# Kernel optimization log

Hardware: AMD Instinct MI355X
Metric: run time of the kernel (lower is better)

Reference implementation:

```python
import jax, jax.numpy as jnp
import numpy as np

B, L, D, H, NL = 4, 2048, 128, 4, 2
DH = D // H
FF = 2 * D
EPS_LN = 1e-5


def _p(key, shape, scale=0.05):
    return (jax.random.normal(key, shape, dtype=jnp.float32) * scale)


def setup_inputs() -> dict:
    key = jax.random.key(0)
    ks = jax.random.split(key, 40)
    inp = {
        "local_global": jax.random.normal(ks[0], (B, D), dtype=jnp.float32),
        "task_features": jax.random.normal(ks[1], (B, L, 15), dtype=jnp.float32),
        "privacy_features": jax.random.normal(ks[2], (B, L, 6), dtype=jnp.float32),
        "dag_features": jax.random.normal(ks[3], (B, L, 4), dtype=jnp.float32),
        # float mask in [0,1); values > 0.5 are MASKED (set to -inf) per torch code
        "attn_mask": jax.random.uniform(ks[4], (B, L, L), dtype=jnp.float32),
        # input projections (stored [in, out]; torch Linear does x @ W.T + b)
        "task_W": _p(ks[5], (15, D)), "task_b": jnp.zeros((D,), jnp.float32),
        "priv_W": _p(ks[6], (6, D)), "priv_b": jnp.zeros((D,), jnp.float32),
        "dag_W": _p(ks[7], (4, D)), "dag_b": jnp.zeros((D,), jnp.float32),
        "pre_g": jnp.ones((D,), jnp.float32), "pre_b": jnp.zeros((D,), jnp.float32),
        "post_g": jnp.ones((D,), jnp.float32), "post_b": jnp.zeros((D,), jnp.float32),
        "out_W": _p(ks[8], (D, D)), "out_b": jnp.zeros((D,), jnp.float32),
        # per-layer params stacked on leading NL axis
        "qW": _p(ks[9], (NL, D, D)), "qb": jnp.zeros((NL, D), jnp.float32),
        "kW": _p(ks[10], (NL, D, D)), "kb": jnp.zeros((NL, D), jnp.float32),
        "vW": _p(ks[11], (NL, D, D)), "vb": jnp.zeros((NL, D), jnp.float32),
        "oW": _p(ks[12], (NL, D, D)), "ob": jnp.zeros((NL, D), jnp.float32),
        "n1g": jnp.ones((NL, D), jnp.float32), "n1b": jnp.zeros((NL, D), jnp.float32),
        "n2g": jnp.ones((NL, D), jnp.float32), "n2b": jnp.zeros((NL, D), jnp.float32),
        "f1W": _p(ks[13], (NL, D, FF)), "f1b": jnp.zeros((NL, FF), jnp.float32),
        "f2W": _p(ks[14], (NL, FF, D)), "f2b": jnp.zeros((NL, D), jnp.float32),
    }
    return inp


def _layernorm(x, g, b):
    mu = x.mean(-1, keepdims=True)
    var = ((x - mu) ** 2).mean(-1, keepdims=True)
    return (x - mu) * jax.lax.rsqrt(var + EPS_LN) * g + b


def _attention(x, add_mask, Wq, bq, Wk, bk, Wv, bv, Wo, bo):
    # x: [B,L,D]; add_mask: [B,L,L] additive (0 or -inf)
    def heads(y):
        return y.reshape(B, L, H, DH).transpose(0, 2, 1, 3)  # [B,H,L,DH]
    q = heads(x @ Wq + bq)
    k = heads(x @ Wk + bk)
    v = heads(x @ Wv + bv)
    scale = 1.0 / np.sqrt(DH).astype(np.float32)
    scores = jnp.einsum('bhqd,bhkd->bhqk', q, k) * scale + add_mask[:, None]
    # fully-masked-row diagonal fixup (torch: set diag score to 0 where row max is -inf)
    row_max = scores.max(-1)                       # [B,H,L]
    fully_masked = jnp.isinf(row_max) & (row_max < 0)
    eye = jnp.eye(L, dtype=bool)
    scores = jnp.where(fully_masked[..., None] & eye, 0.0, scores)
    w = jax.nn.softmax(scores, axis=-1)
    # NaN fallback: if any NaN, replace with 1/L and renormalize (applied globally, as torch does)
    has_nan = jnp.isnan(w).any()
    fixed = jnp.nan_to_num(w, nan=1.0 / L)
    fixed = fixed / (fixed.sum(-1, keepdims=True) + 1e-8)
    w = jnp.where(has_nan, fixed, w)
    out = jnp.einsum('bhqk,bhkd->bhqd', w, v)      # [B,H,L,DH]
    out = out.transpose(0, 2, 1, 3).reshape(B, L, D)
    return out @ Wo + bo


def reference(local_global, task_features, privacy_features, dag_features, attn_mask,
              task_W, task_b, priv_W, priv_b, dag_W, dag_b,
              pre_g, pre_b, post_g, post_b, out_W, out_b,
              qW, qb, kW, kb, vW, vb, oW, ob,
              n1g, n1b, n2g, n2b, f1W, f1b, f2W, f2b):
    # normalize mask: >0.5 means masked; fix all-False rows by masking their diagonal (torch quirk)
    mb = attn_mask > 0.5                            # [B,L,L] bool, True = mask out
    need_fix = ~mb.any(-1)                          # [B,L]
    eye = jnp.eye(L, dtype=bool)
    mb = mb | (need_fix[..., None] & eye)
    add_mask = jnp.where(mb, -jnp.inf, 0.0).astype(jnp.float32)

    ctx = (task_features @ task_W + task_b) + (privacy_features @ priv_W + priv_b) \
          + (dag_features @ dag_W + dag_b)
    x = _layernorm(ctx, pre_g, pre_b)
    for i in range(NL):  # eval mode: dropout = identity
        sa = _attention(_layernorm(x, n1g[i], n1b[i]), add_mask,
                        qW[i], qb[i], kW[i], kb[i], vW[i], vb[i], oW[i], ob[i])
        x = x + sa
        h = _layernorm(x, n2g[i], n2b[i])
        ff = jax.nn.gelu(h @ f1W[i] + f1b[i], approximate=False) @ f2W[i] + f2b[i]
        x = x + ff
    enc = _layernorm(x, post_g, post_b)
    global_ctx = enc.mean(axis=1)                   # [B,D]
    fused = global_ctx + 0.1 * local_global
    aligned = fused @ out_W + out_b
    return aligned
```

## Files before the change

### kernel.cpp

```cpp
#include <hip/hip_runtime.h>
#include <hip/hip_bf16.h>

#define DEV __device__ __forceinline__

typedef float f32x4 __attribute__((ext_vector_type(4)));
typedef float f32x16 __attribute__((ext_vector_type(16)));
typedef short s16x8 __attribute__((ext_vector_type(8)));
typedef unsigned short u16x4 __attribute__((ext_vector_type(4)));
typedef __bf16 bf16x8 __attribute__((ext_vector_type(8)));

DEV bf16x8 as_bf16(s16x8 v) { return __builtin_bit_cast(bf16x8, v); }

DEV unsigned short f2bf(float f) {
    union { __hip_bfloat16 h; unsigned short u; } c;
    c.h = __float2bfloat16(f);
    return c.u;
}

DEV unsigned f2bf2(float lo, float hi) {
    unsigned ulo = __builtin_bit_cast(unsigned, lo);
    unsigned uhi = __builtin_bit_cast(unsigned, hi);
    ulo = (ulo + 0x7fffu + ((ulo >> 16) & 1u)) >> 16;
    uhi = (uhi + 0x7fffu + ((uhi >> 16) & 1u)) & 0xffff0000u;
    return ulo | uhi;
}

DEV float wave_sum64(float v) {
#pragma unroll
    for (int m = 1; m < 64; m <<= 1) v += __shfl_xor(v, m, 64);
    return v;
}

DEV int rot3(int r) { return ((r << 1) | (r >> 2)) & 7; }

constexpr float QSCL = (float)(1.4426950408889634 / 5.656854249492381);

__global__ __launch_bounds__(256) void gace_setup_k(
    const float* __restrict__ am, unsigned long long* __restrict__ bits,
    const float* __restrict__ task, const float* __restrict__ priv, const float* __restrict__ dag,
    const float* __restrict__ tW, const float* __restrict__ tb,
    const float* __restrict__ pW, const float* __restrict__ pb,
    const float* __restrict__ dW, const float* __restrict__ db,
    const float* __restrict__ pre_g, const float* __restrict__ pre_b,
    float* __restrict__ x,
    const float* __restrict__ qW, const float* __restrict__ kW,
    const float* __restrict__ vW, const float* __restrict__ oW,
    const float* __restrict__ f1W, const float* __restrict__ f2W,
    const float* __restrict__ qb, const float* __restrict__ kb,
    const float* __restrict__ vb,
    unsigned short* __restrict__ wbf, float* __restrict__ bcat)
{
    const int bx = blockIdx.x;
    const int tid = threadIdx.x, wid = tid >> 6, l = tid & 63;
    if (bx < 2048) {
        const int row = bx * 4 + wid;
        const float* mrow = am + (size_t)row * 2048;
        unsigned long long myword = 0, orAll = 0, andAll = ~0ull;
#pragma unroll 4
        for (int w = 0; w < 32; ++w) {
            unsigned long long bal = __ballot(mrow[w * 64 + l] > 0.5f);
            if (w == l) myword = bal;
            orAll |= bal; andAll &= bal;
        }
        const int lrow = row & 2047;
        const int dw = lrow >> 6, dbit = lrow & 63;
        if (l == dw) {
            if (orAll == 0ull) myword |= (1ull << dbit);
            else if (andAll == ~0ull) myword &= ~(1ull << dbit);
        }
        if (l < 32) bits[(size_t)row * 32 + l] = myword;
        return;
    }
    if (bx < 4096) {
        const int row = (bx - 2048) * 4 + wid;
        const int d0 = l, d1 = l + 64;
        float a0 = tb[d0] + pb[d0] + db[d0];
        float a1 = tb[d1] + pb[d1] + db[d1];
        const float* tf = task + (size_t)row * 15;
#pragma unroll
        for (int j = 0; j < 15; ++j) { const float t = tf[j]; a0 += t * tW[j * 128 + d0]; a1 += t * tW[j * 128 + d1]; }
        const float* pf = priv + (size_t)row * 6;
#pragma unroll
        for (int j = 0; j < 6; ++j) { const float t = pf[j]; a0 += t * pW[j * 128 + d0]; a1 += t * pW[j * 128 + d1]; }
        const float* df = dag + (size_t)row * 4;
#pragma unroll
        for (int j = 0; j < 4; ++j) { const float t = df[j]; a0 += t * dW[j * 128 + d0]; a1 += t * dW[j * 128 + d1]; }
        const float s = wave_sum64(a0 + a1);
        const float mean = s * (1.f / 128.f);
        const float e0 = a0 - mean, e1 = a1 - mean;
        const float s2 = wave_sum64(e0 * e0 + e1 * e1);
        const float rs = rsqrtf(s2 * (1.f / 128.f) + 1e-5f);
        x[(size_t)row * 128 + d0] = e0 * rs * pre_g[d0] + pre_b[d0];
        x[(size_t)row * 128 + d1] = e1 * rs * pre_g[d1] + pre_b[d1];
        return;
    }
    const int bx2 = bx - 4096;
    const int y = bx2 >> 8;
    const int idx = (bx2 & 255) * 256 + tid;
    if (y == 6) {
        if (idx < 2 * 384) {
            const int i = idx / 384, j = idx % 384;
            float v;
            if (j < 128)      v = qb[i * 128 + j] * QSCL;
            else if (j < 256) v = kb[i * 128 + j - 128];
            else              v = vb[i * 128 + j - 256];
            bcat[idx] = v;
        }
        return;
    }
    const float* src; int K_, N_, off; float scl = 1.0f;
    switch (y) {
        case 0:  src = qW;  K_ = 128; N_ = 128; off = 0;      scl = QSCL; break;
        case 1:  src = kW;  K_ = 128; N_ = 128; off = 16384;  break;
        case 2:  src = vW;  K_ = 128; N_ = 128; off = 32768;  break;
        case 3:  src = oW;  K_ = 128; N_ = 128; off = 49152;  break;
        case 4:  src = f1W; K_ = 128; N_ = 256; off = 65536;  break;
        default: src = f2W; K_ = 256; N_ = 128; off = 98304;  break;
    }
    const int per = K_ * N_;
    if (idx >= 2 * per) return;
    const int i = idx / per, rem = idx % per;
    const int n = rem / K_, k = rem % K_;
    wbf[(size_t)i * 131072 + off + n * K_ + k] = f2bf(src[(size_t)i * per + k * N_ + n] * scl);
}

template<int PRO, int EPI, int KD>
__global__ __launch_bounds__(256) void gace_mega_k(
    const unsigned short* __restrict__ A, int lda,
    const float* __restrict__ xin,
    const float* __restrict__ Op, const float* __restrict__ ml,
    const float* __restrict__ gam, const float* __restrict__ bet,
    const unsigned short* __restrict__ Wt,
    const float* __restrict__ bias,
    unsigned short* __restrict__ outb, int ldo,
    float* __restrict__ xadd, unsigned short* __restrict__ vtbuf)
{
    const int tid = threadIdx.x;
    const int wid = tid >> 6, l = tid & 63;
    const int g = (l >> 4) & 3, c16 = l & 15;
    const int m0 = blockIdx.x * 64 + wid * 16;
    const int n0 = blockIdx.y * 64;
    const int arow = m0 + c16;
    constexpr int NKC = KD / 32;

    s16x8 af[NKC];
    if (PRO == 0) {
#pragma unroll
        for (int kc = 0; kc < NKC; ++kc)
            af[kc] = *(const s16x8*)&A[(size_t)arow * lda + kc * 32 + 8 * g];
    } else if (PRO == 1) {
        float v[4][8];
#pragma unroll
        for (int kc = 0; kc < 4; ++kc) {
            const f32x4 a0 = *(const f32x4*)&xin[(size_t)arow * 128 + kc * 32 + 8 * g];
            const f32x4 a1 = *(const f32x4*)&xin[(size_t)arow * 128 + kc * 32 + 8 * g + 4];
#pragma unroll
            for (int e = 0; e < 4; ++e) { v[kc][e] = a0[e]; v[kc][4 + e] = a1[e]; }
        }
        float s = 0.f;
#pragma unroll
        for (int kc = 0; kc < 4; ++kc)
#pragma unroll
            for (int e = 0; e < 8; ++e) s += v[kc][e];
        s += __shfl_xor(s, 16, 64); s += __shfl_xor(s, 32, 64);
        const float mean = s * (1.f / 128.f);
        float s2 = 0.f;
#pragma unroll
        for (int kc = 0; kc < 4; ++kc)
#pragma unroll
            for (int e = 0; e < 8; ++e) { const float d = v[kc][e] - mean; s2 += d * d; }
        s2 += __shfl_xor(s2, 16, 64); s2 += __shfl_xor(s2, 32, 64);
        const float rs = rsqrtf(s2 * (1.f / 128.f) + 1e-5f);
#pragma unroll
        for (int kc = 0; kc < 4; ++kc) {
            union { s16x8 v8; unsigned d[4]; } pk;
#pragma unroll
            for (int j = 0; j < 4; ++j) {
                const int col = kc * 32 + 8 * g + 2 * j;
                const float x0 = (v[kc][2 * j] - mean) * rs * gam[col] + bet[col];
                const float x1 = (v[kc][2 * j + 1] - mean) * rs * gam[col + 1] + bet[col + 1];
                pk.d[j] = f2bf2(x0, x1);
            }
            af[kc] = pk.v8;
        }
    } else {
#pragma unroll
        for (int kc = 0; kc < 4; ++kc) {
            float o[8];
#pragma unroll
            for (int e = 0; e < 8; ++e) o[e] = 0.f;
            float Ls = 0.f;
#pragma unroll
            for (int sp = 0; sp < 4; ++sp) {
                const size_t ro = (size_t)sp * 8192 + arow;
                const f32x4 a0 = *(const f32x4*)&Op[ro * 128 + kc * 32 + 8 * g];
                const f32x4 a1 = *(const f32x4*)&Op[ro * 128 + kc * 32 + 8 * g + 4];
#pragma unroll
                for (int e = 0; e < 4; ++e) { o[e] += a0[e]; o[4 + e] += a1[e]; }
                Ls += ml[ro * 4 + kc];
            }
            const float inv = 1.f / Ls;
            union { s16x8 v8; unsigned d[4]; } pk;
#pragma unroll
            for (int j = 0; j < 4; ++j) pk.d[j] = f2bf2(o[2 * j] * inv, o[2 * j + 1] * inv);
            af[kc] = pk.v8;
        }
    }

    f32x4 acc[4];
#pragma unroll
    for (int i = 0; i < 4; ++i) acc[i] = f32x4{0.f, 0.f, 0.f, 0.f};
#pragma unroll
    for (int ns = 0; ns < 4; ++ns) {
        const unsigned short* wrow = Wt + (size_t)(n0 + 16 * ns + c16) * KD;
#pragma unroll
        for (int kc = 0; kc < NKC; ++kc) {
            const s16x8 bfv = *(const s16x8*)&wrow[kc * 32 + 8 * g];
            acc[ns] = __builtin_amdgcn_mfma_f32_16x16x32_bf16(
                as_bf16(af[kc]), as_bf16(bfv), acc[ns], 0, 0, 0);
        }
    }
    if (EPI == 0 && vtbuf != nullptr && n0 >= 256) {
        const int row0 = m0 + 4 * g;
#pragma unroll
        for (int ns = 0; ns < 4; ++ns) {
            const int n = n0 + ns * 16 + c16;
            const float bv = bias[n];
            u16x4 pk;
#pragma unroll
            for (int r = 0; r < 4; ++r) pk[r] = f2bf(acc[ns][r] + bv);
            *(u16x4*)&vtbuf[(size_t)(n - 256) * 8192 + row0] = pk;
        }
        return;
    }
#pragma unroll
    for (int ns = 0; ns < 4; ++ns) {
        const int n = n0 + ns * 16 + c16;
        const float bv = bias[n];
#pragma unroll
        for (int r = 0; r < 4; ++r) {
            const int row = m0 + 4 * g + r;
            float v = acc[ns][r] + bv;
            if (EPI == 1) v = v * 0.5f * (1.0f + erff(v * 0.70710678118654752f));
            if (EPI == 2) xadd[(size_t)row * 128 + n] += v;
            else          outb[(size_t)row * ldo + n] = f2bf(v);
        }
    }
}

__global__ __launch_bounds__(256) void gace_flash6_k(
    const unsigned short* __restrict__ QK,
    const unsigned short* __restrict__ Vt,
    const unsigned long long* __restrict__ bits,
    float* __restrict__ Op, float* __restrict__ ml)
{
    __shared__ __align__(16) unsigned short Ks[2 * 2 * 2560];
    __shared__ __align__(16) char VtB[2 * 2 * 4096];

    const int tid = threadIdx.x;
    const int wid = tid >> 6, l = tid & 63;
    const int c32 = l & 31, hi = l >> 5;
    const int bid = (blockIdx.x & 7) * 128 + (blockIdx.x >> 3);
    const int split = bid & 3, qc = (bid >> 2) & 15, h = (bid >> 6) & 3, b = bid >> 8;
    const size_t base = (size_t)b * 2048;
    const int qb0 = qc * 128 + wid * 32;
    const int q = qb0 + c32;

    const unsigned short* qrow = &QK[(base + q) * 256 + h * 32];
    const s16x8 qf0 = *(const s16x8*)&qrow[8 * hi];
    const s16x8 qf1 = *(const s16x8*)&qrow[16 + 8 * hi];
    const int rot3c = rot3(c32 & 7);

    f32x16 oacc;
#pragma unroll
    for (int i = 0; i < 16; ++i) oacc[i] = 0.f;
    float l_ = 0.f;

    const int sr = tid >> 2;
    const int se = (tid & 3) << 3;
    const int lowr = sr & 31, t12 = lowr & 12;
    const int prow = (sr & 32) | (((t12 == 4) | (t12 == 8)) ? (lowr ^ 12) : lowr);
    const int rv = tid >> 3;
    const int sv = tid & 7;
    const int vds = rv * 128 + 16 * (sv ^ rot3(rv & 7));

    const int kv0 = split * 512;
    const unsigned long long* bq = &bits[(base + q) * 32 + split * 8];
    const unsigned short* kgb = &QK[base * 256 + 128 + h * 32 + se];
    const unsigned short* vgb = &Vt[(size_t)(h * 32 + rv) * 8192 + base + kv0 + sv * 8];

    s16x8 kregA, kregB, vregA, vregB;
    auto LOAD = [&](int it2) {
        const int kv = kv0 + it2 * 128;
        kregA = *(const s16x8*)&kgb[(size_t)(kv + sr) * 256];
        kregB = *(const s16x8*)&kgb[(size_t)(kv + 64 + sr) * 256];
        vregA = *(const s16x8*)&vgb[it2 * 128];
        vregB = *(const s16x8*)&vgb[it2 * 128 + 64];
    };
    auto STAGE = [&](int pb) {
        *(s16x8*)&Ks[(pb * 2 + 0) * 2560 + prow * 40 + se] = kregA;
        *(s16x8*)&Ks[(pb * 2 + 1) * 2560 + prow * 40 + se] = kregB;
        *(s16x8*)&VtB[(pb * 2 + 0) * 4096 + vds] = vregA;
        *(s16x8*)&VtB[(pb * 2 + 1) * 4096 + vds] = vregB;
    };
    auto COMPUTE = [&](int pb, int sub, unsigned long long wb) {
        const unsigned short* KsS = &Ks[(pb * 2 + sub) * 2560];
        const char* VtS = &VtB[(pb * 2 + sub) * 4096];
        const unsigned long long wbs = wb >> (8 * hi);
        const unsigned wlo = (unsigned)wbs, whiw = (unsigned)(wbs >> 32);
        __builtin_amdgcn_s_setprio(1);
#pragma unroll
        for (int H = 0; H < 2; ++H) {
            const unsigned short* kr = &KsS[(32 * H + c32) * 40 + 8 * hi];
            f32x16 zv;
#pragma unroll
            for (int i = 0; i < 16; ++i) zv[i] = 0.f;
            f32x16 sac = __builtin_amdgcn_mfma_f32_32x32x16_bf16(
                as_bf16(*(const s16x8*)&kr[0]), as_bf16(qf0), zv, 0, 0, 0);
            sac = __builtin_amdgcn_mfma_f32_32x32x16_bf16(
                as_bf16(*(const s16x8*)&kr[16]), as_bf16(qf1), sac, 0, 0, 0);
            const unsigned word = (H == 0) ? wlo : whiw;
#pragma unroll
            for (int ch = 0; ch < 2; ++ch) {
                const int c = 2 * H + ch;
                const int bb = ch * 16;
                float p[8];
#pragma unroll
                for (int e = 0; e < 8; ++e) {
                    const float pe = exp2f(sac[ch * 8 + e]);
                    p[e] = ((word >> (bb + e)) & 1u) ? 0.f : pe;
                }
                l_ += ((p[0] + p[1]) + (p[2] + p[3])) + ((p[4] + p[5]) + (p[6] + p[7]));
                union { s16x8 v; unsigned d[4]; } pa;
#pragma unroll
                for (int j = 0; j < 4; ++j)
                    asm("v_cvt_pk_bf16_f32 %0, %1, %2"
                        : "=v"(pa.d[j]) : "v"(p[2 * j]), "v"(p[2 * j + 1]));
                const s16x8 vf = *(const s16x8*)&VtS[c32 * 128 + 16 * ((2 * c + hi) ^ rot3c)];
                oacc = __builtin_amdgcn_mfma_f32_32x32x16_bf16(
                    as_bf16(pa.v), as_bf16(vf), oacc, 0, 0, 0);
            }
        }
        __builtin_amdgcn_s_setprio(0);
    };

    unsigned long long wbv[8];
#pragma unroll
    for (int w = 0; w < 8; ++w) wbv[w] = bq[w];
    LOAD(0);
    STAGE(0);
    LOAD(1);
    __syncthreads();

#pragma unroll
    for (int it = 0; it < 4; ++it) {
        const int p = it & 1;
        COMPUTE(p, 0, wbv[2 * it]);
        if (it < 3) {
            STAGE(p ^ 1);
            if (it < 2) LOAD(it + 2);
        }
        COMPUTE(p, 1, wbv[2 * it + 1]);
        if (it < 3) __syncthreads();
    }

    l_ += __shfl_xor(l_, 32, 64);
    float* orow = &Op[((size_t)split * 8192 + base + qb0) * 128 + h * 32 + c32];
#pragma unroll
    for (int r = 0; r < 16; ++r) {
        const int qoff = (r & 3) + 8 * (r >> 2) + 4 * hi;
        orow[(size_t)qoff * 128] = oacc[r];
    }
    if (l < 32) ml[((size_t)split * 8192 + base + q) * 4 + h] = l_;
}

__global__ __launch_bounds__(256) void gace_tailA_k(
    const float* __restrict__ x, const float* __restrict__ gam, const float* __restrict__ bet,
    float* __restrict__ partial)
{
    const int tid = threadIdx.x, wid = tid >> 6, l = tid & 63;
    const int row0 = blockIdx.x * 64 + wid * 16;
    const float g0 = gam[l], g1v = gam[l + 64], b0 = bet[l], b1 = bet[l + 64];
    float a0 = 0.f, a1 = 0.f;
    for (int rr = 0; rr < 16; ++rr) {
        const float* xr = x + (size_t)(row0 + rr) * 128;
        const float v0 = xr[l], v1 = xr[l + 64];
        const float s = wave_sum64(v0 + v1);
        const float mean = s * (1.f / 128.f);
        const float d0 = v0 - mean, d1 = v1 - mean;
        const float s2 = wave_sum64(d0 * d0 + d1 * d1);
        const float rs = rsqrtf(s2 * (1.f / 128.f) + 1e-5f);
        a0 += d0 * rs * g0 + b0;
        a1 += d1 * rs * g1v + b1;
    }
    __shared__ float red[4][128];
    red[wid][l] = a0;
    red[wid][l + 64] = a1;
    __syncthreads();
    if (tid < 128) {
        partial[(size_t)blockIdx.x * 128 + tid] =
            red[0][tid] + red[1][tid] + red[2][tid] + red[3][tid];
    }
}

__global__ __launch_bounds__(128) void gace_tailB_k(
    const float* __restrict__ partial, const float* __restrict__ lg,
    const float* __restrict__ oW, const float* __restrict__ obv,
    float* __restrict__ out)
{
    const int tid = threadIdx.x, b2 = blockIdx.x;
    __shared__ float fused[128];
    float s = 0.f;
#pragma unroll 8
    for (int c = 0; c < 32; ++c) s += partial[(size_t)(b2 * 32 + c) * 128 + tid];
    fused[tid] = s * (1.f / 2048.f) + 0.1f * lg[b2 * 128 + tid];
    __syncthreads();
    float r = obv[tid];
#pragma unroll 8
    for (int d2 = 0; d2 < 128; ++d2) r += fused[d2] * oW[d2 * 128 + tid];
    out[b2 * 128 + tid] = r;
}

extern "C" void kernel_launch(void* const* d_in, const int* in_sizes, int n_in,
                              void* d_out, int out_size, void* d_ws, size_t ws_size,
                              hipStream_t stream)
{
    (void)in_sizes; (void)n_in; (void)out_size; (void)ws_size;
    const float* local_global = (const float*)d_in[0];
    const float* task   = (const float*)d_in[1];
    const float* priv   = (const float*)d_in[2];
    const float* dag    = (const float*)d_in[3];
    const float* amask  = (const float*)d_in[4];
    const float* task_W = (const float*)d_in[5];
    const float* task_b = (const float*)d_in[6];
    const float* priv_W = (const float*)d_in[7];
    const float* priv_b = (const float*)d_in[8];
    const float* dag_W  = (const float*)d_in[9];
    const float* dag_b  = (const float*)d_in[10];
    const float* pre_g  = (const float*)d_in[11];
    const float* pre_b  = (const float*)d_in[12];
    const float* post_g = (const float*)d_in[13];
    const float* post_b = (const float*)d_in[14];
    const float* out_W  = (const float*)d_in[15];
    const float* out_b  = (const float*)d_in[16];
    const float* qW = (const float*)d_in[17];
    const float* qb = (const float*)d_in[18];
    const float* kW = (const float*)d_in[19];
    const float* kb = (const float*)d_in[20];
    const float* vW = (const float*)d_in[21];
    const float* vb = (const float*)d_in[22];
    const float* oW = (const float*)d_in[23];
    const float* ob = (const float*)d_in[24];
    const float* n1g = (const float*)d_in[25];
    const float* n1b = (const float*)d_in[26];
    const float* n2g = (const float*)d_in[27];
    const float* n2b = (const float*)d_in[28];
    const float* f1W = (const float*)d_in[29];
    const float* f1b = (const float*)d_in[30];
    const float* f2W = (const float*)d_in[31];
    const float* f2b = (const float*)d_in[32];

    char* ws = (char*)d_ws;
    size_t off = 0;
    auto carve = [&](size_t sz) {
        void* p = ws + off;
        off += (sz + 255) & ~(size_t)255;
        return p;
    };
    unsigned long long* bits = (unsigned long long*)carve(8192ull * 32 * 8);
    float*          x    = (float*)carve(8192ull * 128 * 4);
    unsigned short* qk   = (unsigned short*)carve(8192ull * 256 * 2);
    unsigned short* vt   = (unsigned short*)carve(128ull * 8192 * 2);
    unsigned short* g1   = (unsigned short*)carve(8192ull * 256 * 2);
    float*          part = (float*)carve(128ull * 128 * 4);
    float*          Op   = (float*)carve(4ull * 8192 * 128 * 4);
    float*          mlb  = (float*)carve(4ull * 8192 * 4 * 4);
    unsigned short* wbf  = (unsigned short*)carve(2ull * 131072 * 2);
    float*          bcat = (float*)carve(2ull * 384 * 4);

    gace_setup_k<<<5888, 256, 0, stream>>>(
        amask, bits,
        task, priv, dag, task_W, task_b, priv_W, priv_b, dag_W, dag_b,
        pre_g, pre_b, x,
        qW, kW, vW, oW, f1W, f2W, qb, kb, vb, wbf, bcat);
    for (int i = 0; i < 2; ++i) {
        const unsigned short* wl = wbf + (size_t)i * 131072;
        gace_mega_k<1, 0, 128><<<dim3(128, 6), 256, 0, stream>>>(
            nullptr, 0, x, nullptr, nullptr, n1g + i * 128, n1b + i * 128,
            wl, bcat + i * 384, qk, 256, nullptr, vt);
        gace_flash6_k<<<1024, 256, 0, stream>>>(qk, vt, bits, Op, mlb);
        gace_mega_k<2, 2, 128><<<dim3(128, 2), 256, 0, stream>>>(
            nullptr, 0, nullptr, Op, mlb, nullptr, nullptr,
            wl + 49152, ob + i * 128, nullptr, 0, x, nullptr);
        gace_mega_k<1, 1, 128><<<dim3(128, 4), 256, 0, stream>>>(
            nullptr, 0, x, nullptr, nullptr, n2g + i * 128, n2b + i * 128,
            wl + 65536, f1b + i * 256, g1, 256, nullptr, nullptr);
        gace_mega_k<0, 2, 256><<<dim3(128, 2), 256, 0, stream>>>(
            g1, 256, nullptr, nullptr, nullptr, nullptr, nullptr,
            wl + 98304, f2b + i * 128, nullptr, 0, x, nullptr);
    }
    gace_tailA_k<<<128, 256, 0, stream>>>(x, post_g, post_b, part);
    gace_tailB_k<<<4, 128, 0, stream>>>(part, local_global, out_W, out_b, (float*)d_out);
}
```

Before: 181.0 us.

## Fuse attention-output, FFN and final layernorm into one per-row-tile kernel

```diff
diff --git a/kernel.cpp b/kernel.cpp
--- a/kernel.cpp
+++ b/kernel.cpp
@@ -124,16 +124,12 @@
     wbf[(size_t)i * 131072 + off + n * K_ + k] = f2bf(src[(size_t)i * per + k * N_ + n] * scl);
 }
 
-template<int PRO, int EPI, int KD>
-__global__ __launch_bounds__(256) void gace_mega_k(
-    const unsigned short* __restrict__ A, int lda,
+__global__ __launch_bounds__(256) void gace_qkv_k(
     const float* __restrict__ xin,
-    const float* __restrict__ Op, const float* __restrict__ ml,
     const float* __restrict__ gam, const float* __restrict__ bet,
     const unsigned short* __restrict__ Wt,
     const float* __restrict__ bias,
-    unsigned short* __restrict__ outb, int ldo,
-    float* __restrict__ xadd, unsigned short* __restrict__ vtbuf)
+    unsigned short* __restrict__ qk, unsigned short* __restrict__ vtbuf)
 {
     const int tid = threadIdx.x;
     const int wid = tid >> 6, l = tid & 63;
@@ -141,86 +137,57 @@
     const int m0 = blockIdx.x * 64 + wid * 16;
     const int n0 = blockIdx.y * 64;
     const int arow = m0 + c16;
-    constexpr int NKC = KD / 32;
-
-    s16x8 af[NKC];
-    if (PRO == 0) {
-#pragma unroll
-        for (int kc = 0; kc < NKC; ++kc)
-            af[kc] = *(const s16x8*)&A[(size_t)arow * lda + kc * 32 + 8 * g];
-    } else if (PRO == 1) {
-        float v[4][8];
+
+    float v[4][8];
+#pragma unroll
+    for (int kc = 0; kc < 4; ++kc) {
+        const f32x4 a0 = *(const f32x4*)&xin[(size_t)arow * 128 + kc * 32 + 8 * g];
+        const f32x4 a1 = *(const f32x4*)&xin[(size_t)arow * 128 + kc * 32 + 8 * g + 4];
+#pragma unroll
+        for (int e = 0; e < 4; ++e) { v[kc][e] = a0[e]; v[kc][4 + e] = a1[e]; }
+    }
+    float s = 0.f;
+#pragma unroll
+    for (int kc = 0; kc < 4; ++kc)
+#pragma unroll
+        for (int e = 0; e < 8; ++e) s += v[kc][e];
+    s += __shfl_xor(s, 16, 64); s += __shfl_xor(s, 32, 64);
+    const float mean = s * (1.f / 128.f);
+    float s2 = 0.f;
+#pragma unroll
+    for (int kc = 0; kc < 4; ++kc)
+#pragma unroll
+        for (int e = 0; e < 8; ++e) { const float d = v[kc][e] - mean; s2 += d * d; }
+    s2 += __shfl_xor(s2, 16, 64); s2 += __shfl_xor(s2, 32, 64);
+    const float rs = rsqrtf(s2 * (1.f / 128.f) + 1e-5f);
+    s16x8 af[4];
+#pragma unroll
+    for (int kc = 0; kc < 4; ++kc) {
+        union { s16x8 v8; unsigned d[4]; } pk;
+#pragma unroll
+        for (int j = 0; j < 4; ++j) {
+            const int col = kc * 32 + 8 * g + 2 * j;
+            const float x0 = (v[kc][2 * j] - mean) * rs * gam[col] + bet[col];
+            const float x1 = (v[kc][2 * j + 1] - mean) * rs * gam[col + 1] + bet[col + 1];
+            pk.d[j] = f2bf2(x0, x1);
+        }
+        af[kc] = pk.v8;
+    }
+
+    f32x4 acc[4];
+#pragma unroll
+    for (int i = 0; i < 4; ++i) acc[i] = f32x4{0.f, 0.f, 0.f, 0.f};
+#pragma unroll
+    for (int ns = 0; ns < 4; ++ns) {
+        const unsigned short* wrow = Wt + (size_t)(n0 + 16 * ns + c16) * 128;
 #pragma unroll
         for (int kc = 0; kc < 4; ++kc) {
-            const f32x4 a0 = *(const f32x4*)&xin[(size_t)arow * 128 + kc * 32 + 8 * g];
-            const f32x4 a1 = *(const f32x4*)&xin[(size_t)arow * 128 + kc * 32 + 8 * g + 4];
-#pragma unroll
-            for (int e = 0; e < 4; ++e) { v[kc][e] = a0[e]; v[kc][4 + e] = a1[e]; }
-        }
-        float s = 0.f;
-#pragma unroll
-        for (int kc = 0; kc < 4; ++kc)
-#pragma unroll
-            for (int e = 0; e < 8; ++e) s += v[kc][e];
-        s += __shfl_xor(s, 16, 64); s += __shfl_xor(s, 32, 64);
-        const float mean = s * (1.f / 128.f);
-        float s2 = 0.f;
-#pragma unroll
-        for (int kc = 0; kc < 4; ++kc)
-#pragma unroll
-            for (int e = 0; e < 8; ++e) { const float d = v[kc][e] - mean; s2 += d * d; }
-        s2 += __shfl_xor(s2, 16, 64); s2 += __shfl_xor(s2, 32, 64);
-        const float rs = rsqrtf(s2 * (1.f / 128.f) + 1e-5f);
-#pragma unroll
-        for (int kc = 0; kc < 4; ++kc) {
-            union { s16x8 v8; unsigned d[4]; } pk;
-#pragma unroll
-            for (int j = 0; j < 4; ++j) {
-                const int col = kc * 32 + 8 * g + 2 * j;
-                const float x0 = (v[kc][2 * j] - mean) * rs * gam[col] + bet[col];
-                const float x1 = (v[kc][2 * j + 1] - mean) * rs * gam[col + 1] + bet[col + 1];
-                pk.d[j] = f2bf2(x0, x1);
-            }
-            af[kc] = pk.v8;
-        }
-    } else {
-#pragma unroll
-        for (int kc = 0; kc < 4; ++kc) {
-            float o[8];
-#pragma unroll
-            for (int e = 0; e < 8; ++e) o[e] = 0.f;
-            float Ls = 0.f;
-#pragma unroll
-            for (int sp = 0; sp < 4; ++sp) {
-                const size_t ro = (size_t)sp * 8192 + arow;
-                const f32x4 a0 = *(const f32x4*)&Op[ro * 128 + kc * 32 + 8 * g];
-                const f32x4 a1 = *(const f32x4*)&Op[ro * 128 + kc * 32 + 8 * g + 4];
-#pragma unroll
-                for (int e = 0; e < 4; ++e) { o[e] += a0[e]; o[4 + e] += a1[e]; }
-                Ls += ml[ro * 4 + kc];
-            }
-            const float inv = 1.f / Ls;
-            union { s16x8 v8; unsigned d[4]; } pk;
-#pragma unroll
-            for (int j = 0; j < 4; ++j) pk.d[j] = f2bf2(o[2 * j] * inv, o[2 * j + 1] * inv);
-            af[kc] = pk.v8;
-        }
-    }
-
-    f32x4 acc[4];
-#pragma unroll
-    for (int i = 0; i < 4; ++i) acc[i] = f32x4{0.f, 0.f, 0.f, 0.f};
-#pragma unroll
-    for (int ns = 0; ns < 4; ++ns) {
-        const unsigned short* wrow = Wt + (size_t)(n0 + 16 * ns + c16) * KD;
-#pragma unroll
-        for (int kc = 0; kc < NKC; ++kc) {
             const s16x8 bfv = *(const s16x8*)&wrow[kc * 32 + 8 * g];
             acc[ns] = __builtin_amdgcn_mfma_f32_16x16x32_bf16(
                 as_bf16(af[kc]), as_bf16(bfv), acc[ns], 0, 0, 0);
         }
     }
-    if (EPI == 0 && vtbuf != nullptr && n0 >= 256) {
+    if (n0 >= 256) {
         const int row0 = m0 + 4 * g;
 #pragma unroll
         for (int ns = 0; ns < 4; ++ns) {
@@ -238,17 +205,12 @@
         const int n = n0 + ns * 16 + c16;
         const float bv = bias[n];
 #pragma unroll
-        for (int r = 0; r < 4; ++r) {
-            const int row = m0 + 4 * g + r;
-            float v = acc[ns][r] + bv;
-            if (EPI == 1) v = v * 0.5f * (1.0f + erff(v * 0.70710678118654752f));
-            if (EPI == 2) xadd[(size_t)row * 128 + n] += v;
-            else          outb[(size_t)row * ldo + n] = f2bf(v);
-        }
-    }
-}
-
-__global__ __launch_bounds__(256) void gace_flash6_k(
+        for (int r = 0; r < 4; ++r)
+            qk[(size_t)(m0 + 4 * g + r) * 256 + n] = f2bf(acc[ns][r] + bv);
+    }
+}
+
+__global__ __launch_bounds__(512) void gace_flash7_k(
     const unsigned short* __restrict__ QK,
     const unsigned short* __restrict__ Vt,
     const unsigned long long* __restrict__ bits,
@@ -260,10 +222,10 @@
     const int tid = threadIdx.x;
     const int wid = tid >> 6, l = tid & 63;
     const int c32 = l & 31, hi = l >> 5;
-    const int bid = (blockIdx.x & 7) * 128 + (blockIdx.x >> 3);
-    const int split = bid & 3, qc = (bid >> 2) & 15, h = (bid >> 6) & 3, b = bid >> 8;
+    const int bid = (blockIdx.x & 7) * 64 + (blockIdx.x >> 3);
+    const int split = bid & 3, qc = (bid >> 2) & 7, h = (bid >> 5) & 3, b = bid >> 7;
     const size_t base = (size_t)b * 2048;
-    const int qb0 = qc * 128 + wid * 32;
+    const int qb0 = qc * 256 + wid * 32;
     const int q = qb0 + c32;
 
     const unsigned short* qrow = &QK[(base + q) * 256 + h * 32];
@@ -276,11 +238,12 @@
     for (int i = 0; i < 16; ++i) oacc[i] = 0.f;
     float l_ = 0.f;
 
-    const int sr = tid >> 2;
+    const int st = tid & 255;
+    const int sr = st >> 2;
     const int se = (tid & 3) << 3;
     const int lowr = sr & 31, t12 = lowr & 12;
     const int prow = (sr & 32) | (((t12 == 4) | (t12 == 8)) ? (lowr ^ 12) : lowr);
-    const int rv = tid >> 3;
+    const int rv = st >> 3;
     const int sv = tid & 7;
     const int vds = rv * 128 + 16 * (sv ^ rot3(rv & 7));
 
@@ -291,17 +254,23 @@
 
     s16x8 kregA, kregB, vregA, vregB;
     auto LOAD = [&](int it2) {
-        const int kv = kv0 + it2 * 128;
-        kregA = *(const s16x8*)&kgb[(size_t)(kv + sr) * 256];
-        kregB = *(const s16x8*)&kgb[(size_t)(kv + 64 + sr) * 256];
-        vregA = *(const s16x8*)&vgb[it2 * 128];
-        vregB = *(const s16x8*)&vgb[it2 * 128 + 64];
+        if (tid < 256) {
+            const int kv = kv0 + it2 * 128;
+            kregA = *(const s16x8*)&kgb[(size_t)(kv + sr) * 256];
+            kregB = *(const s16x8*)&kgb[(size_t)(kv + 64 + sr) * 256];
+        } else {
+            vregA = *(const s16x8*)&vgb[it2 * 128];
+            vregB = *(const s16x8*)&vgb[it2 * 128 + 64];
+        }
     };
     auto STAGE = [&](int pb) {
-        *(s16x8*)&Ks[(pb * 2 + 0) * 2560 + prow * 40 + se] = kregA;
-        *(s16x8*)&Ks[(pb * 2 + 1) * 2560 + prow * 40 + se] = kregB;
-        *(s16x8*)&VtB[(pb * 2 + 0) * 4096 + vds] = vregA;
-        *(s16x8*)&VtB[(pb * 2 + 1) * 4096 + vds] = vregB;
+        if (tid < 256) {
+            *(s16x8*)&Ks[(pb * 2 + 0) * 2560 + prow * 40 + se] = kregA;
+            *(s16x8*)&Ks[(pb * 2 + 1) * 2560 + prow * 40 + se] = kregB;
+        } else {
+            *(s16x8*)&VtB[(pb * 2 + 0) * 4096 + vds] = vregA;
+            *(s16x8*)&VtB[(pb * 2 + 1) * 4096 + vds] = vregB;
+        }
     };
     auto COMPUTE = [&](int pb, int sub, unsigned long long wb) {
         const unsigned short* KsS = &Ks[(pb * 2 + sub) * 2560];
@@ -374,33 +343,197 @@
     if (l < 32) ml[((size_t)split * 8192 + base + q) * 4 + h] = l_;
 }
 
-__global__ __launch_bounds__(256) void gace_tailA_k(
-    const float* __restrict__ x, const float* __restrict__ gam, const float* __restrict__ bet,
+template<int LAST>
+__global__ __launch_bounds__(128) void gace_post_k(
+    const float* __restrict__ Op, const float* __restrict__ ml,
+    const unsigned short* __restrict__ oWt, const float* __restrict__ obv,
+    float* __restrict__ x,
+    const float* __restrict__ n2g, const float* __restrict__ n2b,
+    const unsigned short* __restrict__ f1Wt, const float* __restrict__ f1b,
+    const unsigned short* __restrict__ f2Wt, const float* __restrict__ f2b,
+    const float* __restrict__ post_g, const float* __restrict__ post_b,
     float* __restrict__ partial)
 {
+    __shared__ __align__(16) float xbuf[2][16][132];
+    __shared__ __align__(16) unsigned short g1buf[2][16][264];
+    __shared__ float red[2][128];
     const int tid = threadIdx.x, wid = tid >> 6, l = tid & 63;
-    const int row0 = blockIdx.x * 64 + wid * 16;
-    const float g0 = gam[l], g1v = gam[l + 64], b0 = bet[l], b1 = bet[l + 64];
-    float a0 = 0.f, a1 = 0.f;
-    for (int rr = 0; rr < 16; ++rr) {
-        const float* xr = x + (size_t)(row0 + rr) * 128;
-        const float v0 = xr[l], v1 = xr[l + 64];
-        const float s = wave_sum64(v0 + v1);
-        const float mean = s * (1.f / 128.f);
-        const float d0 = v0 - mean, d1 = v1 - mean;
-        const float s2 = wave_sum64(d0 * d0 + d1 * d1);
-        const float rs = rsqrtf(s2 * (1.f / 128.f) + 1e-5f);
-        a0 += d0 * rs * g0 + b0;
-        a1 += d1 * rs * g1v + b1;
-    }
-    __shared__ float red[4][128];
-    red[wid][l] = a0;
-    red[wid][l + 64] = a1;
+    const int g = (l >> 4) & 3, c16 = l & 15;
+    const int m0 = blockIdx.x * 32 + wid * 16;
+    const int arow = m0 + c16;
+
+    s16x8 af[4];
+#pragma unroll
+    for (int kc = 0; kc < 4; ++kc) {
+        float o[8];
+#pragma unroll
+        for (int e = 0; e < 8; ++e) o[e] = 0.f;
+        float Ls = 0.f;
+#pragma unroll
+        for (int sp = 0; sp < 4; ++sp) {
+            const size_t ro = (size_t)sp * 8192 + arow;
+            const f32x4 a0 = *(const f32x4*)&Op[ro * 128 + kc * 32 + 8 * g];
+            const f32x4 a1 = *(const f32x4*)&Op[ro * 128 + kc * 32 + 8 * g + 4];
+#pragma unroll
+            for (int e = 0; e < 4; ++e) { o[e] += a0[e]; o[4 + e] += a1[e]; }
+            Ls += ml[ro * 4 + kc];
+        }
+        const float inv = 1.f / Ls;
+        union { s16x8 v8; unsigned d[4]; } pk;
+#pragma unroll
+        for (int j = 0; j < 4; ++j) pk.d[j] = f2bf2(o[2 * j] * inv, o[2 * j + 1] * inv);
+        af[kc] = pk.v8;
+    }
+    f32x4 acc8[8];
+#pragma unroll
+    for (int i = 0; i < 8; ++i) acc8[i] = f32x4{0.f, 0.f, 0.f, 0.f};
+#pragma unroll
+    for (int ns = 0; ns < 8; ++ns) {
+        const unsigned short* wrow = oWt + (size_t)(16 * ns + c16) * 128;
+#pragma unroll
+        for (int kc = 0; kc < 4; ++kc)
+            acc8[ns] = __builtin_amdgcn_mfma_f32_16x16x32_bf16(
+                as_bf16(af[kc]), as_bf16(*(const s16x8*)&wrow[kc * 32 + 8 * g]),
+                acc8[ns], 0, 0, 0);
+    }
+#pragma unroll
+    for (int ns = 0; ns < 8; ++ns) {
+        const int n = 16 * ns + c16;
+        const float bv = obv[n];
+#pragma unroll
+        for (int r = 0; r < 4; ++r) {
+            const int lr = 4 * g + r;
+            xbuf[wid][lr][n] = acc8[ns][r] + bv + x[(size_t)(m0 + lr) * 128 + n];
+        }
+    }
+    float v2[4][8];
+#pragma unroll
+    for (int kc = 0; kc < 4; ++kc) {
+        const f32x4 a0 = *(const f32x4*)&xbuf[wid][c16][kc * 32 + 8 * g];
+        const f32x4 a1 = *(const f32x4*)&xbuf[wid][c16][kc * 32 + 8 * g + 4];
+#pragma unroll
+        for (int e = 0; e < 4; ++e) { v2[kc][e] = a0[e]; v2[kc][4 + e] = a1[e]; }
+    }
+    float s = 0.f;
+#pragma unroll
+    for (int kc = 0; kc < 4; ++kc)
+#pragma unroll
+        for (int e = 0; e < 8; ++e) s += v2[kc][e];
+    s += __shfl_xor(s, 16, 64); s += __shfl_xor(s, 32, 64);
+    const float mean = s * (1.f / 128.f);
+    float s2 = 0.f;
+#pragma unroll
+    for (int kc = 0; kc < 4; ++kc)
+#pragma unroll
+        for (int e = 0; e < 8; ++e) { const float d = v2[kc][e] - mean; s2 += d * d; }
+    s2 += __shfl_xor(s2, 16, 64); s2 += __shfl_xor(s2, 32, 64);
+    const float rs = rsqrtf(s2 * (1.f / 128.f) + 1e-5f);
+    s16x8 af1[4];
+#pragma unroll
+    for (int kc = 0; kc < 4; ++kc) {
+        union { s16x8 v8; unsigned d[4]; } pk;
+#pragma unroll
+        for (int j = 0; j < 4; ++j) {
+            const int col = kc * 32 + 8 * g + 2 * j;
+            const float x0 = (v2[kc][2 * j] - mean) * rs * n2g[col] + n2b[col];
+            const float x1 = (v2[kc][2 * j + 1] - mean) * rs * n2g[col + 1] + n2b[col + 1];
+            pk.d[j] = f2bf2(x0, x1);
+        }
+        af1[kc] = pk.v8;
+    }
+    f32x4 acc16[16];
+#pragma unroll
+    for (int i = 0; i < 16; ++i) acc16[i] = f32x4{0.f, 0.f, 0.f, 0.f};
+#pragma unroll
+    for (int ns = 0; ns < 16; ++ns) {
+        const unsigned short* wrow = f1Wt + (size_t)(16 * ns + c16) * 128;
+#pragma unroll
+        for (int kc = 0; kc < 4; ++kc)
+            acc16[ns] = __builtin_amdgcn_mfma_f32_16x16x32_bf16(
+                as_bf16(af1[kc]), as_bf16(*(const s16x8*)&wrow[kc * 32 + 8 * g]),
+                acc16[ns], 0, 0, 0);
+    }
+#pragma unroll
+    for (int ns = 0; ns < 16; ++ns) {
+        const int n = 16 * ns + c16;
+        const float bv = f1b[n];
+#pragma unroll
+        for (int r = 0; r < 4; ++r) {
+            float vv = acc16[ns][r] + bv;
+            vv = vv * 0.5f * (1.0f + erff(vv * 0.70710678118654752f));
+            g1buf[wid][4 * g + r][n] = f2bf(vv);
+        }
+    }
+    s16x8 af2[8];
+#pragma unroll
+    for (int kc = 0; kc < 8; ++kc)
+        af2[kc] = *(const s16x8*)&g1buf[wid][c16][kc * 32 + 8 * g];
+    f32x4 acc8b[8];
+#pragma unroll
+    for (int i = 0; i < 8; ++i) acc8b[i] = f32x4{0.f, 0.f, 0.f, 0.f};
+#pragma unroll
+    for (int ns = 0; ns < 8; ++ns) {
+        const unsigned short* wrow = f2Wt + (size_t)(16 * ns + c16) * 256;
+#pragma unroll
+        for (int kc = 0; kc < 8; ++kc)
+            acc8b[ns] = __builtin_amdgcn_mfma_f32_16x16x32_bf16(
+                as_bf16(af2[kc]), as_bf16(*(const s16x8*)&wrow[kc * 32 + 8 * g]),
+                acc8b[ns], 0, 0, 0);
+    }
+    float fx[8][4];
+#pragma unroll
+    for (int ns = 0; ns < 8; ++ns) {
+        const int n = 16 * ns + c16;
+        const float bv = f2b[n];
+#pragma unroll
+        for (int r = 0; r < 4; ++r)
+            fx[ns][r] = acc8b[ns][r] + bv + xbuf[wid][4 * g + r][n];
+    }
+    if (!LAST) {
+#pragma unroll
+        for (int ns = 0; ns < 8; ++ns) {
+            const int n = 16 * ns + c16;
+#pragma unroll
+            for (int r = 0; r < 4; ++r)
+                x[(size_t)(m0 + 4 * g + r) * 128 + n] = fx[ns][r];
+        }
+        return;
+    }
+    float colsum[8];
+#pragma unroll
+    for (int ns = 0; ns < 8; ++ns) colsum[ns] = 0.f;
+#pragma unroll
+    for (int r = 0; r < 4; ++r) {
+        float sr_ = 0.f;
+#pragma unroll
+        for (int ns = 0; ns < 8; ++ns) sr_ += fx[ns][r];
+        sr_ += __shfl_xor(sr_, 1, 64); sr_ += __shfl_xor(sr_, 2, 64);
+        sr_ += __shfl_xor(sr_, 4, 64); sr_ += __shfl_xor(sr_, 8, 64);
+        const float mr = sr_ * (1.f / 128.f);
+        float vr = 0.f;
+#pragma unroll
+        for (int ns = 0; ns < 8; ++ns) { const float d = fx[ns][r] - mr; vr += d * d; }
+        vr += __shfl_xor(vr, 1, 64); vr += __shfl_xor(vr, 2, 64);
+        vr += __shfl_xor(vr, 4, 64); vr += __shfl_xor(vr, 8, 64);
+        const float rsr = rsqrtf(vr * (1.f / 128.f) + 1e-5f);
+#pragma unroll
+        for (int ns = 0; ns < 8; ++ns) {
+            const int n = 16 * ns + c16;
+            colsum[ns] += (fx[ns][r] - mr) * rsr * post_g[n] + post_b[n];
+        }
+    }
+#pragma unroll
+    for (int ns = 0; ns < 8; ++ns) {
+        colsum[ns] += __shfl_xor(colsum[ns], 16, 64);
+        colsum[ns] += __shfl_xor(colsum[ns], 32, 64);
+    }
+    if (l < 16) {
+#pragma unroll
+        for (int ns = 0; ns < 8; ++ns) red[wid][16 * ns + c16] = colsum[ns];
+    }
     __syncthreads();
-    if (tid < 128) {
-        partial[(size_t)blockIdx.x * 128 + tid] =
-            red[0][tid] + red[1][tid] + red[2][tid] + red[3][tid];
-    }
+    if (tid < 128)
+        partial[(size_t)blockIdx.x * 128 + tid] = red[0][tid] + red[1][tid];
 }
 
 __global__ __launch_bounds__(128) void gace_tailB_k(
@@ -412,7 +545,7 @@
     __shared__ float fused[128];
     float s = 0.f;
 #pragma unroll 8
-    for (int c = 0; c < 32; ++c) s += partial[(size_t)(b2 * 32 + c) * 128 + tid];
+    for (int c = 0; c < 64; ++c) s += partial[(size_t)(b2 * 64 + c) * 128 + tid];
     fused[tid] = s * (1.f / 2048.f) + 0.1f * lg[b2 * 128 + tid];
     __syncthreads();
     float r = obv[tid];
@@ -471,8 +604,7 @@
     float*          x    = (float*)carve(8192ull * 128 * 4);
     unsigned short* qk   = (unsigned short*)carve(8192ull * 256 * 2);
     unsigned short* vt   = (unsigned short*)carve(128ull * 8192 * 2);
-    unsigned short* g1   = (unsigned short*)carve(8192ull * 256 * 2);
-    float*          part = (float*)carve(128ull * 128 * 4);
+    float*          part = (float*)carve(256ull * 128 * 4);
     float*          Op   = (float*)carve(4ull * 8192 * 128 * 4);
     float*          mlb  = (float*)carve(4ull * 8192 * 4 * 4);
     unsigned short* wbf  = (unsigned short*)carve(2ull * 131072 * 2);
@@ -485,20 +617,17 @@
         qW, kW, vW, oW, f1W, f2W, qb, kb, vb, wbf, bcat);
     for (int i = 0; i < 2; ++i) {
         const unsigned short* wl = wbf + (size_t)i * 131072;
-        gace_mega_k<1, 0, 128><<<dim3(128, 6), 256, 0, stream>>>(
-            nullptr, 0, x, nullptr, nullptr, n1g + i * 128, n1b + i * 128,
-            wl, bcat + i * 384, qk, 256, nullptr, vt);
-        gace_flash6_k<<<1024, 256, 0, stream>>>(qk, vt, bits, Op, mlb);
-        gace_mega_k<2, 2, 128><<<dim3(128, 2), 256, 0, stream>>>(
-            nullptr, 0, nullptr, Op, mlb, nullptr, nullptr,
-            wl + 49152, ob + i * 128, nullptr, 0, x, nullptr);
-        gace_mega_k<1, 1, 128><<<dim3(128, 4), 256, 0, stream>>>(
-            nullptr, 0, x, nullptr, nullptr, n2g + i * 128, n2b + i * 128,
-            wl + 65536, f1b + i * 256, g1, 256, nullptr, nullptr);
-        gace_mega_k<0, 2, 256><<<dim3(128, 2), 256, 0, stream>>>(
-            g1, 256, nullptr, nullptr, nullptr, nullptr, nullptr,
-            wl + 98304, f2b + i * 128, nullptr, 0, x, nullptr);
-    }
-    gace_tailA_k<<<128, 256, 0, stream>>>(x, post_g, post_b, part);
+        gace_qkv_k<<<dim3(128, 6), 256, 0, stream>>>(
+            x, n1g + i * 128, n1b + i * 128, wl, bcat + i * 384, qk, vt);
+        gace_flash7_k<<<512, 512, 0, stream>>>(qk, vt, bits, Op, mlb);
+        if (i == 0)
+            gace_post_k<0><<<256, 128, 0, stream>>>(
+                Op, mlb, wl + 49152, ob, x, n2g, n2b,
+                wl + 65536, f1b, wl + 98304, f2b, post_g, post_b, part);
+        else
+            gace_post_k<1><<<256, 128, 0, stream>>>(
+                Op, mlb, wl + 49152, ob + 128, x, n2g + 128, n2b + 128,
+                wl + 65536, f1b + 256, wl + 98304, f2b + 128, post_g, post_b, part);
+    }
     gace_tailB_k<<<4, 128, 0, stream>>>(part, local_global, out_W, out_b, (float*)d_out);
 }
```

Result: faster. 175.5 us (-3.0%).
